# Kernel optimization log

Hardware: AMD Instinct MI355X
Metric: run time of the kernel (lower is better)

The kernel has to match this reference:

```python
import jax, jax.numpy as jnp
import numpy as np

ODE_UNFOLDS = 6   # ncps LTCCell default
EPS = 1e-8
BATCH = 4096

def _conv(x, w, b, stride, pad):
    y = jax.lax.conv_general_dilated(x, w, (stride, stride), [(pad, pad), (pad, pad)],
                                     dimension_numbers=('NCHW', 'OIHW', 'NCHW'))
    return y + b[None, :, None, None]

def _bn(x, g, bta, m, v):
    # eval-mode batchnorm (running stats)
    inv = g * jax.lax.rsqrt(v + 1e-5)
    return x * inv[None, :, None, None] + (bta - m * inv)[None, :, None, None]

def _maxpool2(x):
    return jax.lax.reduce_window(x, -jnp.inf, jax.lax.max, (1, 1, 2, 2), (1, 1, 2, 2), 'VALID')

def _forward(x, conv1_w, conv1_b, conv2_w, conv2_b, bn2_g, bn2_b, bn2_m, bn2_v,
             conv3_w, conv3_b, conv4_w, conv4_b, bn4_g, bn4_b, bn4_m, bn4_v,
             input_w, input_b, sensory_mu, sensory_sigma, sensory_w, sensory_erev, sensory_mask,
             mu, sigma, w, erev, mask, gleak, vleak, cm, output_w, output_b):
    h = jax.nn.relu(_conv(x, conv1_w, conv1_b, 1, 0))                                            # [B,16,26,26]
    h = jax.nn.relu(_bn(_conv(h, conv2_w, conv2_b, 2, 2), bn2_g, bn2_b, bn2_m, bn2_v))           # [B,32,14,14]
    h = jax.nn.relu(_conv(h, conv3_w, conv3_b, 2, 2))                                            # [B,64,7,7]
    h = _maxpool2(jax.nn.relu(_bn(_conv(h, conv4_w, conv4_b, 2, 2), bn4_g, bn4_b, bn4_m, bn4_v)))  # [B,128,2,2]
    seq = h.reshape(-1, 32, 16)                                                                  # [B,T=32,F=16]
    # --- LTC cell (ncps fused ODE solver) ---
    xin = seq * input_w + input_b                                                                # affine input mapping
    # sensory synapses depend only on the input -> precompute for all timesteps
    sact = jax.nn.softplus(sensory_w) * jax.nn.sigmoid((xin[..., None] - sensory_mu) * sensory_sigma) * sensory_mask  # [B,T,16,19]
    wnum_s = jnp.einsum('btsn,sn->btn', sact, sensory_erev)   # [B,T,19]
    wden_s = jnp.sum(sact, axis=2)                            # [B,T,19]
    w_pos = jax.nn.softplus(w) * mask                         # [pre=19,post=19]
    gl = jax.nn.softplus(gleak)
    cm_t = jax.nn.softplus(cm) * ODE_UNFOLDS                  # cm / (elapsed_time=1.0 / unfolds)
    def tstep(v, nd):
        wns, wds = nd
        def unfold(v2, _):
            wa = w_pos * jax.nn.sigmoid((v2[..., None] - mu) * sigma)   # [B,19,19]
            num = cm_t * v2 + gl * vleak + jnp.sum(wa * erev, axis=1) + wns
            den = cm_t + gl + jnp.sum(wa, axis=1) + wds
            return num / (den + EPS), None
        v, _ = jax.lax.scan(unfold, v, None, length=ODE_UNFOLDS)
        return v, None
    h0 = jnp.zeros((seq.shape[0], 19), seq.dtype)
    vT, _ = jax.lax.scan(tstep, h0, (jnp.swapaxes(wnum_s, 0, 1), jnp.swapaxes(wden_s, 0, 1)))
    # out[:, -1, :] == output mapping of final state; motor neurons are the first 2
    return vT[:, :2] * output_w + output_b


def setup_inputs() -> dict:
    key = jax.random.key(0)
    ks = jax.random.split(key, 16)
    rng = np.random.default_rng(0)
    u = lambda k, s, lo, hi: jax.random.uniform(k, s, jnp.float32, lo, hi)
    n = lambda k, s, sc: jax.random.normal(k, s, jnp.float32) * sc
    inp = {}
    inp['x'] = jax.random.normal(ks[0], (BATCH, 1, 28, 28), jnp.float32)
    inp['conv1_w'] = n(ks[1], (16, 1, 3, 3), 0.3); inp['conv1_b'] = jnp.zeros(16)
    inp['conv2_w'] = n(ks[2], (32, 16, 3, 3), 0.08); inp['conv2_b'] = jnp.zeros(32)
    inp['bn2_g'] = jnp.ones(32); inp['bn2_b'] = jnp.zeros(32)
    inp['bn2_m'] = jnp.zeros(32); inp['bn2_v'] = jnp.ones(32)
    inp['conv3_w'] = n(ks[3], (64, 32, 5, 5), 0.035); inp['conv3_b'] = jnp.zeros(64)
    inp['conv4_w'] = n(ks[4], (128, 64, 5, 5), 0.025); inp['conv4_b'] = jnp.zeros(128)
    inp['bn4_g'] = jnp.ones(128); inp['bn4_b'] = jnp.zeros(128)
    inp['bn4_m'] = jnp.zeros(128); inp['bn4_v'] = jnp.ones(128)
    inp['input_w'] = jnp.ones(16); inp['input_b'] = jnp.zeros(16)
    # ncps LTCCell init ranges
    inp['sensory_mu'] = u(ks[5], (16, 19), 0.3, 0.8)
    inp['sensory_sigma'] = u(ks[6], (16, 19), 3.0, 8.0)
    inp['sensory_w'] = u(ks[7], (16, 19), 0.001, 1.0)
    inp['sensory_erev'] = jnp.asarray(rng.choice([-1.0, 1.0], (16, 19)).astype(np.float32))
    inp['sensory_mask'] = jnp.asarray((rng.random((16, 19)) < 0.35).astype(np.float32))
    inp['mu'] = u(ks[8], (19, 19), 0.3, 0.8)
    inp['sigma'] = u(ks[9], (19, 19), 3.0, 8.0)
    inp['w'] = u(ks[10], (19, 19), 0.001, 1.0)
    inp['erev'] = jnp.asarray(rng.choice([-1.0, 1.0], (19, 19)).astype(np.float32))
    inp['mask'] = jnp.asarray((rng.random((19, 19)) < 0.35).astype(np.float32))
    inp['gleak'] = u(ks[11], (19,), 0.001, 1.0)
    inp['vleak'] = u(ks[12], (19,), -0.2, 0.2)
    inp['cm'] = u(ks[13], (19,), 0.4, 0.6)
    inp['output_w'] = jnp.ones(2); inp['output_b'] = jnp.zeros(2)
    return inp


def reference(x, conv1_w, conv1_b, conv2_w, conv2_b, bn2_g, bn2_b, bn2_m, bn2_v,
              conv3_w, conv3_b, conv4_w, conv4_b, bn4_g, bn4_b, bn4_m, bn4_v,
              input_w, input_b, sensory_mu, sensory_sigma, sensory_w, sensory_erev, sensory_mask,
              mu, sigma, w, erev, mask, gleak, vleak, cm, output_w, output_b):
    return _forward(x, conv1_w, conv1_b, conv2_w, conv2_b, bn2_g, bn2_b, bn2_m, bn2_v,
                    conv3_w, conv3_b, conv4_w, conv4_b, bn4_g, bn4_b, bn4_m, bn4_v,
                    input_w, input_b, sensory_mu, sensory_sigma, sensory_w, sensory_erev, sensory_mask,
                    mu, sigma, w, erev, mask, gleak, vleak, cm, output_w, output_b)
```

## Files before the change

### kernel.cpp

```cpp
#include <hip/hip_runtime.h>

#define BATCH 4096
typedef unsigned short u16_t;

#define P_SWM   0
#define P_SWME  304
#define P_WP    608
#define P_WPE   969
#define P_GL    1330
#define P_GLVL  1349
#define P_CMT   1368
#define P_SC2   1392
#define P_SH2   1424
#define P_SC4   1456
#define P_SH4   1584

#define OFF_PAR 0L
#define OFF_B2F 2048L
#define OFF_B3F 6656L
#define OFF_B4F 57856L
#define OFF_DYN 262656L

typedef __attribute__((ext_vector_type(8))) short short8;
typedef __attribute__((ext_vector_type(16))) float f32x16;
typedef __attribute__((ext_vector_type(4))) float f32x4;
#define MFMA(a, b, c) __builtin_amdgcn_mfma_f32_32x32x16_bf16(a, b, c, 0, 0, 0)
#define MFMA16(a, b, c) __builtin_amdgcn_mfma_f32_16x16x32_bf16(a, b, c, 0, 0, 0)

#define PERM_HI(w1, w0) __builtin_amdgcn_perm((w1), (w0), 0x05040100u)
#define PERM_LO(w1, w0) __builtin_amdgcn_perm((w1), (w0), 0x07060302u)

union U8 { unsigned u[4]; short8 v; };
union A4 { f32x4 v; float f[4]; };

__device__ __forceinline__ float sigmoidf_(float x) {
    return 1.0f / (1.0f + __expf(-x));
}
__device__ __forceinline__ float softplusf_(float x) { return log1pf(__expf(x)); }

__device__ __forceinline__ unsigned splitpack(float f) {
    unsigned u = __float_as_uint(f);
    float rsd = f - __uint_as_float(u & 0xFFFF0000u);
    unsigned ur = __float_as_uint(rsd);
    ur = ur + 0x7FFFu + ((ur >> 16) & 1u);
    return (u >> 16) | (ur & 0xFFFF0000u);
}
__device__ __forceinline__ u16_t bfhalf(float v, int pl) {
    unsigned u = __float_as_uint(v);
    if (pl == 0) return (u16_t)(u >> 16);
    float rsd = v - __uint_as_float(u & 0xFFFF0000u);
    unsigned ur = __float_as_uint(rsd);
    ur = ur + 0x7FFFu + ((ur >> 16) & 1u);
    return (u16_t)(ur >> 16);
}

__global__ __launch_bounds__(256) void k_prep(
    const float* __restrict__ w2, const float* __restrict__ w3, const float* __restrict__ w4,
    const float* __restrict__ sw, const float* __restrict__ serev, const float* __restrict__ smask,
    const float* __restrict__ w,  const float* __restrict__ erev,  const float* __restrict__ mask,
    const float* __restrict__ gleak, const float* __restrict__ vleak, const float* __restrict__ cm,
    const float* __restrict__ b2, const float* __restrict__ g2, const float* __restrict__ be2,
    const float* __restrict__ m2, const float* __restrict__ v2,
    const float* __restrict__ b4, const float* __restrict__ g4, const float* __restrict__ be4,
    const float* __restrict__ m4, const float* __restrict__ v4,
    float* __restrict__ ws) {
    int gid = blockIdx.x * 256 + threadIdx.x, stride = gridDim.x * 256;
    u16_t* b2f = (u16_t*)(ws + OFF_B2F);
    u16_t* b3f = (u16_t*)(ws + OFF_B3F);
    u16_t* b4f = (u16_t*)(ws + OFF_B4F);
    for (int i = gid; i < 9216; i += stride) {
        int j = i & 7, ln = (i >> 3) & 63;
        int r = i >> 9;
        int s = r % 9, pl = r / 9;
        int k = s * 16 + (ln >> 5) * 8 + j;
        int tap = k >> 4, ci = k & 15;
        int co = ln & 31;
        b2f[i] = bfhalf(w2[(co * 16 + ci) * 9 + tap], pl);
    }
    for (int i = gid; i < 102400; i += stride) {
        int j = i & 7, ln = (i >> 3) & 63;
        int t = i >> 9;
        int tap = t % 25, r = t / 25;
        int nt = r & 3, pl = r >> 2;
        int co = nt * 16 + (ln & 15);
        int ci = (ln >> 4) * 8 + j;
        b3f[i] = bfhalf(w3[(co * 32 + ci) * 25 + tap], pl);
    }
    for (int i = gid; i < 409600; i += stride) {
        int j = i & 7, ln = (i >> 3) & 63;
        int t = i >> 9;
        int ks = t % 50, r = t / 50;
        int nt = r & 7, pl = r >> 3;
        int co = nt * 16 + (ln & 15);
        int tap = ks >> 1;
        int ci = (ks & 1) * 32 + (ln >> 4) * 8 + j;
        b4f[i] = bfhalf(w4[(co * 64 + ci) * 25 + tap], pl);
    }
    if (blockIdx.x == 0) {
        float* par = ws + OFF_PAR;
        int tid = threadIdx.x;
        for (int i = tid; i < 304; i += 256) {
            float v_ = softplusf_(sw[i]) * smask[i];
            par[P_SWM + i] = v_;
            par[P_SWME + i] = v_ * serev[i];
        }
        for (int i = tid; i < 361; i += 256) {
            float v_ = softplusf_(w[i]) * mask[i];
            par[P_WP + i] = v_;
            par[P_WPE + i] = v_ * erev[i];
        }
        for (int i = tid; i < 19; i += 256) {
            float g = softplusf_(gleak[i]);
            par[P_GL + i] = g;
            par[P_GLVL + i] = g * vleak[i];
            par[P_CMT + i] = softplusf_(cm[i]) * 6.0f;
        }
        for (int i = tid; i < 32; i += 256) {
            float inv = g2[i] * __frsqrt_rn(v2[i] + 1e-5f);
            par[P_SC2 + i] = inv;
            par[P_SH2 + i] = (b2[i] - m2[i]) * inv + be2[i];
        }
        for (int i = tid; i < 128; i += 256) {
            float inv = g4[i] * __frsqrt_rn(v4[i] + 1e-5f);
            par[P_SC4 + i] = inv;
            par[P_SH4 + i] = (b4[i] - m4[i]) * inv + be4[i];
        }
    }
}

__global__ __launch_bounds__(512, 4) void k_conv12(
    const float* __restrict__ x, const float* __restrict__ w1, const float* __restrict__ b1,
    const float* __restrict__ ws, unsigned* __restrict__ h2g) {
    __shared__ float xs[784];
    __shared__ unsigned h1s[14300];
    const float* par = ws + OFF_PAR;
    int b = blockIdx.x, tid = threadIdx.x;
    {
        for (int i = tid; i < 784; i += 512) xs[i] = x[(long)b * 784 + i];
        uint4* hz = (uint4*)h1s;
        uint4 z; z.x = z.y = z.z = z.w = 0u;
        for (int i = tid; i < 3575; i += 512) hz[i] = z;
    }
    __syncthreads();
    {
        int co = tid >> 5, slot = tid & 31;
        float wr[9];
        #pragma unroll
        for (int i = 0; i < 9; i++) wr[i] = w1[co * 9 + i];
        float bb = b1[co];
        for (int k = 0; k < 22; k++) {
            int px = slot + (k << 5);
            if (px >= 676) break;
            int oh = px / 26, ow = px % 26;
            float s = bb;
            #pragma unroll
            for (int kh = 0; kh < 3; kh++)
                #pragma unroll
                for (int kw = 0; kw < 3; kw++)
                    s = fmaf(xs[(oh + kh) * 28 + ow + kw], wr[kh * 3 + kw], s);
            h1s[((oh + 2) * 29 + (ow + 2)) * 17 + co] = splitpack(fmaxf(s, 0.f));
        }
    }
    __syncthreads();
    {
        int wv = tid >> 6, lane = tid & 63;
        int mloc = lane & 31, hf = lane >> 5, half8 = hf * 8;
        const u16_t* B2 = (const u16_t*)(ws + OFF_B2F);
        const short8* pb = (const short8*)B2 + lane;
        float sc = par[P_SC2 + mloc], sh = par[P_SH2 + mloc];
        int mt = wv;
        if (mt < 7) {
            int px = mt * 32 + mloc;
            bool pxok = px < 196;
            int pxc = pxok ? px : 195;
            int oh = pxc / 14, ow = pxc % 14;
            f32x16 acc;
            #pragma unroll
            for (int i = 0; i < 16; i++) acc[i] = 0.f;
            #pragma unroll
            for (int s = 0; s < 9; s++) {
                int kh = s / 3, kw = s % 3;
                int abase = (pxok ? ((oh * 2 + kh) * 29 + (ow * 2 + kw)) * 17 : 0) + half8;
                unsigned w_[8];
                #pragma unroll
                for (int j = 0; j < 8; j++) w_[j] = h1s[abase + j];
                U8 ah, al;
                #pragma unroll
                for (int d = 0; d < 4; d++) {
                    ah.u[d] = PERM_HI(w_[2 * d + 1], w_[2 * d]);
                    al.u[d] = PERM_LO(w_[2 * d + 1], w_[2 * d]);
                }
                short8 bh = pb[s * 64];
                short8 bl = pb[(9 + s) * 64];
                acc = MFMA(ah.v, bh, acc);
                acc = MFMA(ah.v, bl, acc);
                acc = MFMA(al.v, bh, acc);
            }
            #pragma unroll
            for (int r5 = 0; r5 < 16; r5++) {
                int row = (r5 & 3) + 8 * (r5 >> 2) + 4 * hf;
                int pxw = mt * 32 + row;
                if (pxw < 196) {
                    float y = fmaxf(fmaf(acc[r5], sc, sh), 0.f);
                    h2g[(long)b * 6272 + pxw * 32 + mloc] = splitpack(y);
                }
            }
        }
    }
}

__global__ __launch_bounds__(256, 2) void k_conv34s(
    const unsigned* __restrict__ h2g, const float* __restrict__ b3g,
    const float* __restrict__ inw, const float* __restrict__ inb,
    const float* __restrict__ smu, const float* __restrict__ ssig,
    const float* __restrict__ ws,
    float* __restrict__ wn, float* __restrict__ wd, int nimg) {
    __shared__ unsigned h2s[12969];
    __shared__ unsigned h3s[6435];
    const float* par = ws + OFF_PAR;
    int b = blockIdx.x, tid = threadIdx.x;
    int g0 = b * 2;
    int g1 = (g0 + 1 < nimg) ? g0 + 1 : g0;
    {
        const unsigned* s0 = h2g + (long)g0 * 6272;
        const unsigned* s1 = h2g + (long)g1 * 6272;
        for (int i = tid; i < 12544; i += 256) {
            int img = i >= 6272;
            int r = img ? i - 6272 : i;
            h2s[img * 6468 + (r >> 5) * 33 + (r & 31)] = (img ? s1 : s0)[r];
        }
        if (tid < 33) h2s[12936 + tid] = 0u;
        if (tid < 65) h3s[6370 + tid] = 0u;
    }
    __syncthreads();
    int wv = tid >> 6, lane = tid & 63;
    int n16 = lane & 15, quad = lane >> 4, quad8 = quad * 8;

    {
        int img = wv & 1, mhalf = wv >> 1;
        int imgo = img * 6468;
        int mt0 = mhalf * 2;
        A4 acc[2][4];
        #pragma unroll
        for (int nt = 0; nt < 4; nt++) {
            float bi = b3g[nt * 16 + n16];
            #pragma unroll
            for (int r = 0; r < 4; r++) { acc[0][nt].f[r] = bi; acc[1][nt].f[r] = bi; }
        }
        int oh2[2], ow2[2];
        bool pxok[2];
        #pragma unroll
        for (int mi = 0; mi < 2; mi++) {
            int px = (mt0 + mi) * 16 + n16;
            pxok[mi] = px < 49;
            int pxc = pxok[mi] ? px : 48;
            oh2[mi] = (pxc / 7) * 2 - 2;
            ow2[mi] = (pxc % 7) * 2 - 2;
        }
        const short8* B3 = (const short8*)(const u16_t*)(ws + OFF_B3F);
        const short8* ph0 = B3 + (0 * 25) * 64 + lane;
        const short8* ph1 = B3 + (1 * 25) * 64 + lane;
        const short8* ph2 = B3 + (2 * 25) * 64 + lane;
        const short8* ph3 = B3 + (3 * 25) * 64 + lane;
        const short8* pl0 = B3 + (4 * 25) * 64 + lane;
        const short8* pl1 = B3 + (5 * 25) * 64 + lane;
        const short8* pl2 = B3 + (6 * 25) * 64 + lane;
        const short8* pl3 = B3 + (7 * 25) * 64 + lane;
        #pragma unroll
        for (int kh = 0; kh < 5; kh++) {
            #pragma unroll
            for (int kw = 0; kw < 5; kw++) {
                int s = (kh * 5 + kw) * 64;
                short8 bh0 = ph0[s], bh1 = ph1[s], bh2 = ph2[s], bh3 = ph3[s];
                short8 bl0 = pl0[s], bl1 = pl1[s], bl2 = pl2[s], bl3 = pl3[s];
                #pragma unroll
                for (int mi = 0; mi < 2; mi++) {
                    int ih = oh2[mi] + kh, iw = ow2[mi] + kw;
                    bool ok = pxok[mi] && ((unsigned)ih < 14u) && ((unsigned)iw < 14u);
                    int rowb = ok ? imgo + (ih * 14 + iw) * 33 : 12936;
                    const unsigned* ap = h2s + rowb + quad8;
                    unsigned w_[8];
                    #pragma unroll
                    for (int j = 0; j < 8; j++) w_[j] = ap[j];
                    U8 ah, al;
                    #pragma unroll
                    for (int d = 0; d < 4; d++) {
                        ah.u[d] = PERM_HI(w_[2 * d + 1], w_[2 * d]);
                        al.u[d] = PERM_LO(w_[2 * d + 1], w_[2 * d]);
                    }
                    acc[mi][0].v = MFMA16(ah.v, bh0, acc[mi][0].v);
                    acc[mi][0].v = MFMA16(ah.v, bl0, acc[mi][0].v);
                    acc[mi][0].v = MFMA16(al.v, bh0, acc[mi][0].v);
                    acc[mi][1].v = MFMA16(ah.v, bh1, acc[mi][1].v);
                    acc[mi][1].v = MFMA16(ah.v, bl1, acc[mi][1].v);
                    acc[mi][1].v = MFMA16(al.v, bh1, acc[mi][1].v);
                    acc[mi][2].v = MFMA16(ah.v, bh2, acc[mi][2].v);
                    acc[mi][2].v = MFMA16(ah.v, bl2, acc[mi][2].v);
                    acc[mi][2].v = MFMA16(al.v, bh2, acc[mi][2].v);
                    acc[mi][3].v = MFMA16(ah.v, bh3, acc[mi][3].v);
                    acc[mi][3].v = MFMA16(ah.v, bl3, acc[mi][3].v);
                    acc[mi][3].v = MFMA16(al.v, bh3, acc[mi][3].v);
                }
            }
        }
        #pragma unroll
        for (int mi = 0; mi < 2; mi++) {
            #pragma unroll
            for (int nt = 0; nt < 4; nt++) {
                int co = nt * 16 + n16;
                #pragma unroll
                for (int r = 0; r < 4; r++) {
                    int pxw = (mt0 + mi) * 16 + quad * 4 + r;
                    if (pxw < 49)
                        h3s[img * 3185 + pxw * 65 + co] = splitpack(fmaxf(acc[mi][nt].f[r], 0.f));
                }
            }
        }
    }
    __syncthreads();
    {
        int oh = n16 >> 2, ow = n16 & 3;
        int oh2 = oh * 2 - 2, ow2 = ow * 2 - 2;
        int nt0 = wv * 2, nt1 = nt0 + 1;
        A4 c[2][2];
        #pragma unroll
        for (int mi = 0; mi < 2; mi++)
            #pragma unroll
            for (int r = 0; r < 4; r++) { c[mi][0].f[r] = 0.f; c[mi][1].f[r] = 0.f; }
        const short8* B4 = (const short8*)(const u16_t*)(ws + OFF_B4F);
        const short8* ph0 = B4 + (nt0 * 50) * 64 + lane;
        const short8* ph1 = B4 + (nt1 * 50) * 64 + lane;
        const short8* pl0 = B4 + ((8 + nt0) * 50) * 64 + lane;
        const short8* pl1 = B4 + ((8 + nt1) * 50) * 64 + lane;
        #pragma unroll
        for (int kh = 0; kh < 5; kh++) {
            int ih = oh2 + kh;
            #pragma unroll
            for (int kw = 0; kw < 5; kw++) {
                int iw = ow2 + kw;
                bool ok = ((unsigned)ih < 7u) && ((unsigned)iw < 7u);
                #pragma unroll
                for (int ch = 0; ch < 2; ch++) {
                    int s = ((kh * 5 + kw) * 2 + ch) * 64;
                    short8 bh0 = ph0[s], bl0 = pl0[s];
                    short8 bh1 = ph1[s], bl1 = pl1[s];
                    #pragma unroll
                    for (int mi = 0; mi < 2; mi++) {
                        int rowb = ok ? mi * 3185 + (ih * 7 + iw) * 65 + ch * 32 : 6370;
                        const unsigned* ap = h3s + rowb + quad8;
                        unsigned w_[8];
                        #pragma unroll
                        for (int j = 0; j < 8; j++) w_[j] = ap[j];
                        U8 ah, al;
                        #pragma unroll
                        for (int d = 0; d < 4; d++) {
                            ah.u[d] = PERM_HI(w_[2 * d + 1], w_[2 * d]);
                            al.u[d] = PERM_LO(w_[2 * d + 1], w_[2 * d]);
                        }
                        c[mi][0].v = MFMA16(ah.v, bh0, c[mi][0].v);
                        c[mi][0].v = MFMA16(ah.v, bl0, c[mi][0].v);
                        c[mi][0].v = MFMA16(al.v, bh0, c[mi][0].v);
                        c[mi][1].v = MFMA16(ah.v, bh1, c[mi][1].v);
                        c[mi][1].v = MFMA16(ah.v, bl1, c[mi][1].v);
                        c[mi][1].v = MFMA16(al.v, bh1, c[mi][1].v);
                    }
                }
            }
        }
        __syncthreads();
        float* xin_s = (float*)h2s;
        #pragma unroll
        for (int mi = 0; mi < 2; mi++) {
            #pragma unroll
            for (int t2 = 0; t2 < 2; t2++) {
                int co = (t2 ? nt1 : nt0) * 16 + n16;
                float sc = par[P_SC4 + co], sh = par[P_SH4 + co];
                float y[4];
                #pragma unroll
                for (int r = 0; r < 4; r++) y[r] = fmaxf(fmaf(c[mi][t2].f[r], sc, sh), 0.f);
                float p0 = fmaxf(y[0], y[1]);
                float p1 = fmaxf(y[2], y[3]);
                p0 = fmaxf(p0, __shfl_xor(p0, 16));
                p1 = fmaxf(p1, __shfl_xor(p1, 16));
                if ((quad & 1) == 0) {
                    int ph_ = quad >> 1;
                    int ts = co >> 2;
                    int f0 = ((co & 3) << 2) + ph_ * 2;
                    xin_s[mi * 512 + ts * 16 + f0] = fmaf(p0, inw[f0], inb[f0]);
                    xin_s[mi * 512 + ts * 16 + f0 + 1] = fmaf(p1, inw[f0 + 1], inb[f0 + 1]);
                }
            }
        }
    }
    __syncthreads();
    const float* xin_s = (const float*)h2s;
    for (int idx = tid; idx < 1216; idx += 256) {
        int img = idx >= 608;
        int r = img ? idx - 608 : idx;
        int gi = g0 + img;
        if (gi >= nimg) break;
        int tt = r / 19, n = r - tt * 19;
        float nu = 0.f, de = 0.f;
        #pragma unroll
        for (int s = 0; s < 16; s++) {
            float sg = sigmoidf_((xin_s[img * 512 + tt * 16 + s] - smu[s * 19 + n]) * ssig[s * 19 + n]);
            nu = fmaf(par[P_SWME + s * 19 + n], sg, nu);
            de = fmaf(par[P_SWM + s * 19 + n], sg, de);
        }
        wn[((long)gi * 32 + tt) * 19 + n] = nu;
        wd[((long)gi * 32 + tt) * 19 + n] = de;
    }
}

__global__ __launch_bounds__(256, 2) void k_ltc(
    const float* __restrict__ mu_g, const float* __restrict__ sg_g,
    const float* __restrict__ ws,
    const float* __restrict__ wn, const float* __restrict__ wd,
    const float* __restrict__ outw, const float* __restrict__ outb,
    float* __restrict__ out, int img0, int nimg) {
    const float* par = ws + OFF_PAR;
    int tid = threadIdx.x, wave = tid >> 6, lane = tid & 63;
    int li = lane / 19, j = lane - li * 19;
    if (li > 2) { li = 2; j = 18; }
    int il = blockIdx.x * 12 + wave * 3 + li;
    int ilc = il < nimg ? il : nimg - 1;

    const float L2E = 1.44269504f;
    float aj[19], bj[19], wpj[19], wpej[19];
    #pragma unroll
    for (int i = 0; i < 19; i++) {
        float mu = mu_g[i * 19 + j];
        float sg = sg_g[i * 19 + j];
        aj[i] = -sg * L2E;
        bj[i] = mu * sg * L2E;
        wpj[i] = par[P_WP + i * 19 + j];
        wpej[i] = par[P_WPE + i * 19 + j];
    }
    float cmt = par[P_CMT + j], gl = par[P_GL + j], glvl = par[P_GLVL + j];
    float v = 0.f;
    long base0 = (long)ilc * 608 + j;
    float wns = wn[base0], wds = wd[base0];
    for (int t = 0; t < 32; t++) {
        float wns_n = 0.f, wds_n = 0.f;
        if (t < 31) {
            long basen = base0 + (t + 1) * 19;
            wns_n = wn[basen];
            wds_n = wd[basen];
        }
        #pragma unroll 1
        for (int u = 0; u < 6; u++) {
            float n0 = 0.f, n1 = 0.f, d0 = 0.f, d1 = 0.f;
            #pragma unroll
            for (int i = 0; i < 19; i++) {
                float vi = __shfl(v, li * 19 + i, 64);
                float e = __builtin_amdgcn_exp2f(fmaf(vi, aj[i], bj[i]));
                float s = __builtin_amdgcn_rcpf(1.0f + e);
                if (i & 1) { n1 = fmaf(wpej[i], s, n1); d1 = fmaf(wpj[i], s, d1); }
                else       { n0 = fmaf(wpej[i], s, n0); d0 = fmaf(wpj[i], s, d0); }
            }
            float num = fmaf(cmt, v, glvl) + wns + (n0 + n1);
            float den = cmt + gl + wds + (d0 + d1);
            v = num * __builtin_amdgcn_rcpf(den + 1e-8f);
        }
        wns = wns_n; wds = wds_n;
    }
    if (j < 2 && il < nimg && lane < 57)
        out[(long)(img0 + il) * 2 + j] = fmaf(v, outw[j], outb[j]);
}

extern "C" void kernel_launch(void* const* d_in, const int* in_sizes, int n_in,
                              void* d_out, int out_size, void* d_ws, size_t ws_size,
                              hipStream_t stream) {
    const float* x    = (const float*)d_in[0];
    const float* w1   = (const float*)d_in[1];
    const float* b1   = (const float*)d_in[2];
    const float* w2   = (const float*)d_in[3];
    const float* b2   = (const float*)d_in[4];
    const float* g2   = (const float*)d_in[5];
    const float* be2  = (const float*)d_in[6];
    const float* m2   = (const float*)d_in[7];
    const float* v2   = (const float*)d_in[8];
    const float* w3   = (const float*)d_in[9];
    const float* b3   = (const float*)d_in[10];
    const float* w4   = (const float*)d_in[11];
    const float* b4   = (const float*)d_in[12];
    const float* g4   = (const float*)d_in[13];
    const float* be4  = (const float*)d_in[14];
    const float* m4   = (const float*)d_in[15];
    const float* v4   = (const float*)d_in[16];
    const float* inw  = (const float*)d_in[17];
    const float* inb  = (const float*)d_in[18];
    const float* smu  = (const float*)d_in[19];
    const float* ssig = (const float*)d_in[20];
    const float* sw   = (const float*)d_in[21];
    const float* serv = (const float*)d_in[22];
    const float* smk  = (const float*)d_in[23];
    const float* mu_  = (const float*)d_in[24];
    const float* sig_ = (const float*)d_in[25];
    const float* w_   = (const float*)d_in[26];
    const float* erev = (const float*)d_in[27];
    const float* mask = (const float*)d_in[28];
    const float* glk  = (const float*)d_in[29];
    const float* vlk  = (const float*)d_in[30];
    const float* cm   = (const float*)d_in[31];
    const float* outw = (const float*)d_in[32];
    const float* outb = (const float*)d_in[33];
    float* ws = (float*)d_ws;

    k_prep<<<64, 256, 0, stream>>>(w2, w3, w4, sw, serv, smk, w_, erev, mask,
                                   glk, vlk, cm, b2, g2, be2, m2, v2,
                                   b4, g4, be4, m4, v4, ws);

    long avail = (long)(ws_size / 4) - OFF_DYN;
    long per = 6272 + 1216;
    int chunk = (int)(avail / per);
    if (chunk > BATCH) chunk = BATCH;
    if (chunk < 2) chunk = 2;

    float* wnp = ws + OFF_DYN;
    float* wdp = wnp + (long)chunk * 608;
    unsigned* h2 = (unsigned*)(wdp + (long)chunk * 608);

    for (int c0 = 0; c0 < BATCH; c0 += chunk) {
        int n = (BATCH - c0 < chunk) ? (BATCH - c0) : chunk;
        k_conv12<<<n, 512, 0, stream>>>(x + (long)c0 * 784, w1, b1, ws, h2);
        k_conv34s<<<(n + 1) / 2, 256, 0, stream>>>(h2, b3, inw, inb, smu, ssig, ws,
                                                   wnp, wdp, n);
        k_ltc<<<(n + 11) / 12, 256, 0, stream>>>(mu_, sig_, ws, wnp, wdp, outw, outb,
                                                 (float*)d_out, c0, n);
    }
}
```

Measured before the change: 565.6 us.

## Fuse LTC ODE recurrence into conv3/4 kernel using LDS for sensory terms

Merges the separate LTC kernel into the conv3/4 + sensory kernel: sensory numerator/denominator are kept in shared memory and the first wave runs the 6-unfold ODE over 32 timesteps for the block's two images. This removes a kernel launch and the global write/read of the wn/wd buffers, and frees workspace so the chunk can be larger. In exchange, three of four waves idle during the serial recurrence while the block still holds its large LDS allocation, reducing conv throughput per CU.

```diff
diff --git a/kernel.cpp b/kernel.cpp
--- a/kernel.cpp
+++ b/kernel.cpp
@@ -209,12 +209,14 @@
     }
 }
 
-__global__ __launch_bounds__(256, 2) void k_conv34s(
+__global__ __launch_bounds__(256, 2) void k_conv34l(
     const unsigned* __restrict__ h2g, const float* __restrict__ b3g,
     const float* __restrict__ inw, const float* __restrict__ inb,
     const float* __restrict__ smu, const float* __restrict__ ssig,
+    const float* __restrict__ mu_g, const float* __restrict__ sg_g,
+    const float* __restrict__ outw, const float* __restrict__ outb,
     const float* __restrict__ ws,
-    float* __restrict__ wn, float* __restrict__ wd, int nimg) {
+    float* __restrict__ out, int img0g, int nimg) {
     __shared__ unsigned h2s[12969];
     __shared__ unsigned h3s[6435];
     const float* par = ws + OFF_PAR;
@@ -393,79 +395,71 @@
         }
     }
     __syncthreads();
-    const float* xin_s = (const float*)h2s;
-    for (int idx = tid; idx < 1216; idx += 256) {
-        int img = idx >= 608;
-        int r = img ? idx - 608 : idx;
-        int gi = g0 + img;
-        if (gi >= nimg) break;
-        int tt = r / 19, n = r - tt * 19;
-        float nu = 0.f, de = 0.f;
-        #pragma unroll
-        for (int s = 0; s < 16; s++) {
-            float sg = sigmoidf_((xin_s[img * 512 + tt * 16 + s] - smu[s * 19 + n]) * ssig[s * 19 + n]);
-            nu = fmaf(par[P_SWME + s * 19 + n], sg, nu);
-            de = fmaf(par[P_SWM + s * 19 + n], sg, de);
-        }
-        wn[((long)gi * 32 + tt) * 19 + n] = nu;
-        wd[((long)gi * 32 + tt) * 19 + n] = de;
-    }
-}
-
-__global__ __launch_bounds__(256, 2) void k_ltc(
-    const float* __restrict__ mu_g, const float* __restrict__ sg_g,
-    const float* __restrict__ ws,
-    const float* __restrict__ wn, const float* __restrict__ wd,
-    const float* __restrict__ outw, const float* __restrict__ outb,
-    float* __restrict__ out, int img0, int nimg) {
-    const float* par = ws + OFF_PAR;
-    int tid = threadIdx.x, wave = tid >> 6, lane = tid & 63;
-    int li = lane / 19, j = lane - li * 19;
-    if (li > 2) { li = 2; j = 18; }
-    int il = blockIdx.x * 12 + wave * 3 + li;
-    int ilc = il < nimg ? il : nimg - 1;
-
-    const float L2E = 1.44269504f;
-    float aj[19], bj[19], wpj[19], wpej[19];
-    #pragma unroll
-    for (int i = 0; i < 19; i++) {
-        float mu = mu_g[i * 19 + j];
-        float sg = sg_g[i * 19 + j];
-        aj[i] = -sg * L2E;
-        bj[i] = mu * sg * L2E;
-        wpj[i] = par[P_WP + i * 19 + j];
-        wpej[i] = par[P_WPE + i * 19 + j];
-    }
-    float cmt = par[P_CMT + j], gl = par[P_GL + j], glvl = par[P_GLVL + j];
-    float v = 0.f;
-    long base0 = (long)ilc * 608 + j;
-    float wns = wn[base0], wds = wd[base0];
-    for (int t = 0; t < 32; t++) {
-        float wns_n = 0.f, wds_n = 0.f;
-        if (t < 31) {
-            long basen = base0 + (t + 1) * 19;
-            wns_n = wn[basen];
-            wds_n = wd[basen];
-        }
-        #pragma unroll 1
-        for (int u = 0; u < 6; u++) {
-            float n0 = 0.f, n1 = 0.f, d0 = 0.f, d1 = 0.f;
-            #pragma unroll
-            for (int i = 0; i < 19; i++) {
-                float vi = __shfl(v, li * 19 + i, 64);
-                float e = __builtin_amdgcn_exp2f(fmaf(vi, aj[i], bj[i]));
-                float s = __builtin_amdgcn_rcpf(1.0f + e);
-                if (i & 1) { n1 = fmaf(wpej[i], s, n1); d1 = fmaf(wpj[i], s, d1); }
-                else       { n0 = fmaf(wpej[i], s, n0); d0 = fmaf(wpj[i], s, d0); }
-            }
-            float num = fmaf(cmt, v, glvl) + wns + (n0 + n1);
-            float den = cmt + gl + wds + (d0 + d1);
-            v = num * __builtin_amdgcn_rcpf(den + 1e-8f);
-        }
-        wns = wns_n; wds = wds_n;
-    }
-    if (j < 2 && il < nimg && lane < 57)
-        out[(long)(img0 + il) * 2 + j] = fmaf(v, outw[j], outb[j]);
+    {
+        const float* xin_s = (const float*)h2s;
+        float* wnl = (float*)h2s + 1024;
+        float* wdl = wnl + 1216;
+        for (int idx = tid; idx < 1216; idx += 256) {
+            int img = idx >= 608;
+            int r = img ? idx - 608 : idx;
+            int tt = r / 19, n = r - tt * 19;
+            float nu = 0.f, de = 0.f;
+            #pragma unroll
+            for (int s = 0; s < 16; s++) {
+                float sg = sigmoidf_((xin_s[img * 512 + tt * 16 + s] - smu[s * 19 + n]) * ssig[s * 19 + n]);
+                nu = fmaf(par[P_SWME + s * 19 + n], sg, nu);
+                de = fmaf(par[P_SWM + s * 19 + n], sg, de);
+            }
+            wnl[img * 608 + r] = nu;
+            wdl[img * 608 + r] = de;
+        }
+    }
+    __syncthreads();
+    if (tid >= 64) return;
+    {
+        int li = tid / 19, j = tid - li * 19;
+        if (li > 1) { li = 1; j = 18; }
+        const float L2E = 1.44269504f;
+        float aj[19], bj[19], wpj[19], wpej[19];
+        #pragma unroll
+        for (int i = 0; i < 19; i++) {
+            float mu = mu_g[i * 19 + j];
+            float sg = sg_g[i * 19 + j];
+            aj[i] = -sg * L2E;
+            bj[i] = mu * sg * L2E;
+            wpj[i] = par[P_WP + i * 19 + j];
+            wpej[i] = par[P_WPE + i * 19 + j];
+        }
+        float cmt = par[P_CMT + j], gl = par[P_GL + j], glvl = par[P_GLVL + j];
+        const float* wnl = (const float*)h2s + 1024;
+        const float* wdl = wnl + 1216;
+        int base = li * 608 + j;
+        float v = 0.f;
+        for (int t = 0; t < 32; t++) {
+            float wns = wnl[base + t * 19];
+            float wds = wdl[base + t * 19];
+            #pragma unroll 1
+            for (int u = 0; u < 6; u++) {
+                float n0 = 0.f, n1 = 0.f, d0 = 0.f, d1 = 0.f;
+                #pragma unroll
+                for (int i = 0; i < 19; i++) {
+                    float vi = __shfl(v, li * 19 + i, 64);
+                    float e = __builtin_amdgcn_exp2f(fmaf(vi, aj[i], bj[i]));
+                    float s = __builtin_amdgcn_rcpf(1.0f + e);
+                    if (i & 1) { n1 = fmaf(wpej[i], s, n1); d1 = fmaf(wpj[i], s, d1); }
+                    else       { n0 = fmaf(wpej[i], s, n0); d0 = fmaf(wpj[i], s, d0); }
+                }
+                float num = fmaf(cmt, v, glvl) + wns + (n0 + n1);
+                float den = cmt + gl + wds + (d0 + d1);
+                v = num * __builtin_amdgcn_rcpf(den + 1e-8f);
+            }
+        }
+        if (j < 2 && tid < 38) {
+            int gi = g0 + li;
+            if (gi < nimg)
+                out[(long)(img0g + gi) * 2 + j] = fmaf(v, outw[j], outb[j]);
+        }
+    }
 }
 
 extern "C" void kernel_launch(void* const* d_in, const int* in_sizes, int n_in,
@@ -512,21 +506,17 @@
                                    b4, g4, be4, m4, v4, ws);
 
     long avail = (long)(ws_size / 4) - OFF_DYN;
-    long per = 6272 + 1216;
-    int chunk = (int)(avail / per);
+    int chunk = (int)(avail / 6272);
     if (chunk > BATCH) chunk = BATCH;
     if (chunk < 2) chunk = 2;
 
-    float* wnp = ws + OFF_DYN;
-    float* wdp = wnp + (long)chunk * 608;
-    unsigned* h2 = (unsigned*)(wdp + (long)chunk * 608);
+    unsigned* h2 = (unsigned*)(ws + OFF_DYN);
 
     for (int c0 = 0; c0 < BATCH; c0 += chunk) {
         int n = (BATCH - c0 < chunk) ? (BATCH - c0) : chunk;
         k_conv12<<<n, 512, 0, stream>>>(x + (long)c0 * 784, w1, b1, ws, h2);
-        k_conv34s<<<(n + 1) / 2, 256, 0, stream>>>(h2, b3, inw, inb, smu, ssig, ws,
-                                                   wnp, wdp, n);
-        k_ltc<<<(n + 11) / 12, 256, 0, stream>>>(mu_, sig_, ws, wnp, wdp, outw, outb,
-                                                 (float*)d_out, c0, n);
-    }
-}
+        k_conv34l<<<(n + 1) / 2, 256, 0, stream>>>(h2, b3, inw, inb, smu, ssig,
+                                                   mu_, sig_, outw, outb, ws,
+                                                   (float*)d_out, c0, n);
+    }
+}
```

Result: slower. 800.7 us (+41.6%).
